# Kernel tuning notes

Measured on AMD Instinct MI355X. Metric: run time of the kernel, lower is better.

The kernel has to match this reference:

```python
import jax, jax.numpy as jnp
import numpy as np

B, S, D, H, ROT = 2, 2048, 2048, 16, 64
HD = D // H  # 128


def setup_inputs() -> dict:
    key = jax.random.key(0)
    ks = jax.random.split(key, 6)
    sc = 0.02
    return {
        "hidden_states": jax.random.normal(ks[0], (B, S, D), jnp.float32),
        "attention_mask": jnp.zeros((B, 1, 1, S), jnp.float32),  # HF additive mask; 0 == keep
        "position_ids": jnp.tile(jnp.arange(S, dtype=jnp.int32), (B, 1)),
        "Wq": jax.random.normal(ks[1], (D, D), jnp.float32) * sc,
        "Wk": jax.random.normal(ks[2], (D, D), jnp.float32) * sc,
        "Wv": jax.random.normal(ks[3], (D, D), jnp.float32) * sc,
        "Wo": jax.random.normal(ks[4], (D, D), jnp.float32) * sc,
        "norm_const": 0.5 * jnp.ones((1, H, 1, 1), jnp.float32),
    }


def _rotate_every_two(x):
    x1 = x[..., ::2]
    x2 = x[..., 1::2]
    return jnp.stack((-x2, x1), axis=-1).reshape(x.shape)


def _apply_rope(x, sin, cos):
    # x: [B,S,H,ROT]; sin/cos: [B,S,ROT//2] -> repeat_interleave(2) as in GPT-J
    sin2 = jnp.repeat(sin, 2, axis=-1)[:, :, None, :]
    cos2 = jnp.repeat(cos, 2, axis=-1)[:, :, None, :]
    return x * cos2 + _rotate_every_two(x) * sin2


def reference(hidden_states, attention_mask, position_ids, Wq, Wk, Wv, Wo, norm_const):
    # projections (nn.Linear, no bias): y = x @ W^T
    q = (hidden_states @ Wq.T).reshape(B, S, H, HD)
    k = (hidden_states @ Wk.T).reshape(B, S, H, HD)
    v = (hidden_states @ Wv.T).reshape(B, S, H, HD).transpose(0, 2, 1, 3)  # [B,H,S,HD]

    # GPT-J sinusoidal rotary on first ROT dims
    inv_freq = 1.0 / (10000.0 ** (jnp.arange(0, ROT, 2, dtype=jnp.float32) / ROT))
    ang = position_ids.astype(jnp.float32)[:, :, None] * inv_freq  # [B,S,ROT//2]
    sin, cos = jnp.sin(ang), jnp.cos(ang)
    q = jnp.concatenate([_apply_rope(q[..., :ROT], sin, cos), q[..., ROT:]], axis=-1)
    k = jnp.concatenate([_apply_rope(k[..., :ROT], sin, cos), k[..., ROT:]], axis=-1)
    q = q.transpose(0, 2, 1, 3)  # [B,H,S,HD]
    k = k.transpose(0, 2, 1, 3)

    # cosine attention: L2-normalize q and k (F.normalize, eps=1e-12)
    eps = 1e-12
    qn = q / jnp.clip(jnp.linalg.norm(q, axis=-1, keepdims=True), eps)
    kn = k / jnp.clip(jnp.linalg.norm(k, axis=-1, keepdims=True), eps)

    keep = attention_mask == 0                               # [B,1,1,S] bool
    causal = jnp.tril(jnp.ones((S, S), bool))[None, None]    # [1,1,S,S]
    # per-query count of visible keys -> value rescale with learned exponent
    counts = jnp.sum((causal & keep).astype(jnp.float32), axis=-1, keepdims=True)  # [B,1,S,1]
    expo = jax.nn.sigmoid(norm_const)                        # [1,H,1,1]
    v = v / jnp.clip(counts ** expo, 1.0)                    # [B,H,S,HD]

    keep_t = jnp.swapaxes(keep, -1, -2).astype(q.dtype)      # [B,1,S,1]
    qn = qn * keep_t
    kn = kn * keep_t
    v = v * keep_t

    attn = jnp.einsum('bhqd,bhkd->bhqk', qn, kn)             # cosine scores
    attn = jnp.where(causal, attn, 0.0)                      # causal zero-mask (no softmax)
    out = jnp.einsum('bhqk,bhkd->bhqd', attn, v)             # [B,H,S,HD]
    out = out.transpose(0, 2, 1, 3).reshape(B, S, D)
    return out @ Wo.T
```

## Files before the change

kernel.cpp:

```cpp
#include <hip/hip_runtime.h>
#include <hip/hip_bf16.h>

typedef __attribute__((ext_vector_type(8))) short bf16x8;
typedef __attribute__((ext_vector_type(4))) float f32x4;
typedef unsigned short u16;
typedef unsigned int u32;

constexpr int B = 2, S = 2048, D = 2048, H = 16, HD = 128, ROT = 64;
constexpr int NQKV = 3 * D;

__device__ __forceinline__ void gload16(const u16* g, u16* l)
{
    __builtin_amdgcn_global_load_lds((const __attribute__((address_space(1))) void*)g,
                                     (__attribute__((address_space(3))) void*)l, 16, 0, 0);
}

__device__ __forceinline__ float bf2f(u32 lo16) { return __uint_as_float(lo16 << 16); }

__global__ void cast_kernel(const float* __restrict__ in, u16* __restrict__ out, int n4)
{
    int idx = blockIdx.x * blockDim.x + threadIdx.x;
    int stride = gridDim.x * blockDim.x;
    for (int i = idx; i < n4; i += stride) {
        float4 v = ((const float4*)in)[i];
        __hip_bfloat16 a = __float2bfloat16(v.x);
        __hip_bfloat16 b = __float2bfloat16(v.y);
        __hip_bfloat16 c = __float2bfloat16(v.z);
        __hip_bfloat16 d = __float2bfloat16(v.w);
        ushort4 o;
        o.x = *(u16*)&a; o.y = *(u16*)&b; o.z = *(u16*)&c; o.w = *(u16*)&d;
        ((ushort4*)out)[i] = o;
    }
}

__global__ void castw_kernel(const float* __restrict__ w0, const float* __restrict__ w1,
                             const float* __restrict__ w2, const float* __restrict__ w3,
                             u16* __restrict__ o0, u16* __restrict__ o1,
                             u16* __restrict__ o2, u16* __restrict__ o3, int n4)
{
    int which = blockIdx.y;
    const float* src = which == 0 ? w0 : which == 1 ? w1 : which == 2 ? w2 : w3;
    u16* dst = which == 0 ? o0 : which == 1 ? o1 : which == 2 ? o2 : o3;
    int idx = blockIdx.x * blockDim.x + threadIdx.x;
    int stride = gridDim.x * blockDim.x;
    for (int i = idx; i < n4; i += stride) {
        float4 v = ((const float4*)src)[i];
        __hip_bfloat16 a = __float2bfloat16(v.x);
        __hip_bfloat16 b = __float2bfloat16(v.y);
        __hip_bfloat16 c = __float2bfloat16(v.z);
        __hip_bfloat16 d = __float2bfloat16(v.w);
        ushort4 o;
        o.x = *(u16*)&a; o.y = *(u16*)&b; o.z = *(u16*)&c; o.w = *(u16*)&d;
        ((ushort4*)dst)[i] = o;
    }
}

__global__ void prep_kernel(const float* __restrict__ mask, const int* __restrict__ pos,
                            const float* __restrict__ ncst,
                            float* __restrict__ sinb, float* __restrict__ cosb,
                            float* __restrict__ keep, float* __restrict__ expo)
{
    int gid = blockIdx.x * blockDim.x + threadIdx.x;
    int total = B * S * 32;
    if (gid < total) {
        int j = gid & 31;
        int bs = gid >> 5;
        float p = (float)pos[bs];
        float f = powf(10000.f, -(float)j / 32.f);
        float ang = p * f;
        sinb[gid] = sinf(ang);
        cosb[gid] = cosf(ang);
        if (j == 0) keep[bs] = (mask[bs] == 0.f) ? 1.f : 0.f;
    }
    if (gid < H) expo[gid] = 1.f / (1.f + expf(-ncst[gid]));
}

__global__ void counts_kernel(const float* __restrict__ keep, float* __restrict__ counts)
{
    __shared__ float part[256];
    int b = blockIdx.x, t = threadIdx.x;
    float v[8];
    float s = 0.f;
    const float* kp = keep + b * S + t * 8;
#pragma unroll
    for (int i = 0; i < 8; ++i) { s += kp[i]; v[i] = s; }
    part[t] = s;
    __syncthreads();
    float off = 0.f;
    for (int j = 0; j < t; ++j) off += part[j];
    float* cp = counts + b * S + t * 8;
#pragma unroll
    for (int i = 0; i < 8; ++i) cp[i] = off + v[i];
}


template <int CNT>
__device__ __forceinline__ void stage_op(const u16* __restrict__ G, int K,
                                         int trow0, int kt, u16* lbuf, int tid)
{
#pragma unroll
    for (int l = 0; l < CNT; ++l) {
        int idx = l * 512 + tid;
        int row = idx >> 2;
        int slot = idx & 3;
        int col8 = slot ^ ((row >> 1) & 3);
        const u16* g = G + (size_t)(trow0 + row) * K + kt * 32 + col8 * 8;
        u16* ld = lbuf + (size_t)(idx & ~63) * 8;
        gload16(g, ld);
    }
}

template <int BM, int BN, int CA, int CB, int MR, int NR, int BF16OUT>
__global__ __launch_bounds__(512, 2) void gemm32(
    const u16* __restrict__ A, const u16* __restrict__ Bm,
    float* __restrict__ Cf, u16* __restrict__ Cb, int N, int K, int ntn)
{
    __shared__ u16 As[3 * BM * 32];
    __shared__ u16 Bs[3 * BN * 32];
    const int tid = threadIdx.x;
    const int lane = tid & 63;
    const int w = tid >> 6;
    const int wm = w >> 2;
    const int wn = w & 3;
    const int l15 = lane & 15, l4 = lane >> 4;

    int nwg = gridDim.x;
    int bid = blockIdx.x;
    int cpx = nwg >> 3;
    int sbid = (bid & 7) * cpx + (bid >> 3);
    int bm = sbid / ntn, bn = sbid % ntn;
    const int bmrow = bm * BM, bnrow = bn * BN;

    f32x4 acc[MR][NR] = {};
    const int nk = K >> 5;

    stage_op<CA>(A, K, bmrow, 0, &As[0], tid);
    stage_op<CB>(Bm, K, bnrow, 0, &Bs[0], tid);
    stage_op<CA>(A, K, bmrow, 1, &As[BM * 32], tid);
    stage_op<CB>(Bm, K, bnrow, 1, &Bs[BN * 32], tid);

    int c0 = 0;
    for (int t = 0; t < nk; ++t) {
        const u16* ab = &As[c0 * BM * 32];
        const u16* bb = &Bs[c0 * BN * 32];
        if (t + 2 < nk) {
            int c2 = c0 + 2; if (c2 >= 3) c2 -= 3;
            stage_op<CA>(A, K, bmrow, t + 2, &As[c2 * BM * 32], tid);
            stage_op<CB>(Bm, K, bnrow, t + 2, &Bs[c2 * BN * 32], tid);
            asm volatile("s_waitcnt vmcnt(%0)" :: "i"(2 * (CA + CB)) : "memory");
        } else if (t + 1 < nk) {
            asm volatile("s_waitcnt vmcnt(%0)" :: "i"(CA + CB) : "memory");
        } else {
            asm volatile("s_waitcnt vmcnt(0)" ::: "memory");
        }
        __builtin_amdgcn_sched_barrier(0);
        __builtin_amdgcn_s_barrier();

        bf16x8 af[MR];
#pragma unroll
        for (int i = 0; i < MR; ++i) {
            int row = wm * (BM / 2) + i * 16 + l15;
            int slot = l4 ^ ((row >> 1) & 3);
            af[i] = *(const bf16x8*)(ab + row * 32 + slot * 8);
        }
#pragma unroll
        for (int n = 0; n < NR; ++n) {
            int brow = wn * (BN / 4) + n * 16 + l15;
            int bslot = l4 ^ ((brow >> 1) & 3);
            bf16x8 bf = *(const bf16x8*)(bb + brow * 32 + bslot * 8);
            __builtin_amdgcn_s_setprio(1);
#pragma unroll
            for (int i = 0; i < MR; ++i)
                acc[i][n] = __builtin_amdgcn_mfma_f32_16x16x32_bf16(af[i], bf, acc[i][n], 0, 0, 0);
            __builtin_amdgcn_s_setprio(0);
        }
        __builtin_amdgcn_sched_barrier(0);
        __builtin_amdgcn_s_barrier();
        c0 = (c0 + 1 == 3) ? 0 : c0 + 1;
    }

#pragma unroll
    for (int i = 0; i < MR; ++i) {
        int row = bmrow + wm * (BM / 2) + i * 16 + l4 * 4;
#pragma unroll
        for (int n = 0; n < NR; ++n) {
            int col = bnrow + wn * (BN / 4) + n * 16 + l15;
            f32x4 v = acc[i][n];
#pragma unroll
            for (int r = 0; r < 4; ++r) {
                if (BF16OUT) {
                    __hip_bfloat16 hv = __float2bfloat16(v[r]);
                    Cb[(size_t)(row + r) * N + col] = *(u16*)&hv;
                } else {
                    Cf[(size_t)(row + r) * N + col] = v[r];
                }
            }
        }
    }
}

__global__ void postproc_all(const u16* __restrict__ tmpb,
                             u16* __restrict__ qn, u16* __restrict__ kn, u16* __restrict__ vr,
                             const float* __restrict__ sinb, const float* __restrict__ cosb,
                             const float* __restrict__ keep, const float* __restrict__ counts,
                             const float* __restrict__ expo)
{
    int gw = (blockIdx.x * blockDim.x + threadIdx.x) >> 6;
    int lane = threadIdx.x & 63;
    if (gw >= B * S * H) return;
    int h = gw % H;
    int sb = gw / H;
    int s = sb % S;
    int b = sb / S;
    const u16* rowp = tmpb + (size_t)(b * S + s) * NQKV;
    u32 qv = *(const u32*)(rowp + h * 128 + lane * 2);
    u32 kv = *(const u32*)(rowp + D + h * 128 + lane * 2);
    u32 vv = *(const u32*)(rowp + 2 * D + h * 128 + lane * 2);
    float q0 = bf2f(qv & 0xffff), q1 = bf2f(qv >> 16);
    float k0 = bf2f(kv & 0xffff), k1 = bf2f(kv >> 16);
    float v0 = bf2f(vv & 0xffff), v1 = bf2f(vv >> 16);
    if (lane < 32) {
        float sn = sinb[(b * S + s) * 32 + lane];
        float cs = cosb[(b * S + s) * 32 + lane];
        float nq0 = q0 * cs - q1 * sn, nq1 = q1 * cs + q0 * sn;
        float nk0 = k0 * cs - k1 * sn, nk1 = k1 * cs + k0 * sn;
        q0 = nq0; q1 = nq1; k0 = nk0; k1 = nk1;
    }
    float sq = q0 * q0 + q1 * q1;
    float sk = k0 * k0 + k1 * k1;
#pragma unroll
    for (int o = 1; o < 64; o <<= 1) {
        sq += __shfl_xor(sq, o, 64);
        sk += __shfl_xor(sk, o, 64);
    }
    float kf = keep[b * S + s];
    float scq = kf / fmaxf(sqrtf(sq), 1e-12f);
    float sck = kf / fmaxf(sqrtf(sk), 1e-12f);
    float cnt = counts[b * S + s];
    float e = expo[h];
    float scv = kf / fmaxf(powf(cnt, e), 1.0f);

    __hip_bfloat16 a0 = __float2bfloat16(q0 * scq), a1 = __float2bfloat16(q1 * scq);
    __hip_bfloat16 b0 = __float2bfloat16(k0 * sck), b1 = __float2bfloat16(k1 * sck);
    __hip_bfloat16 c0 = __float2bfloat16(v0 * scv), c1 = __float2bfloat16(v1 * scv);
    size_t obase = ((size_t)(b * H + h) * S + s) * 128 + lane * 2;
    *(u32*)(qn + obase) = (u32)*(u16*)&a0 | ((u32)*(u16*)&a1 << 16);
    *(u32*)(kn + obase) = (u32)*(u16*)&b0 | ((u32)*(u16*)&b1 << 16);
    *(u32*)(vr + obase) = (u32)*(u16*)&c0 | ((u32)*(u16*)&c1 << 16);
}

__global__ __launch_bounds__(256) void chunk_state(
    const u16* __restrict__ kn, const u16* __restrict__ vr, u16* __restrict__ T16)
{
    __shared__ u16 As[128][72];
    __shared__ u16 Bs[128][72];
    int tid = threadIdx.x, lane = tid & 63, w = tid >> 6;
    int wm = w >> 1, wn = w & 1;
    int c = blockIdx.x, bh = blockIdx.y;
    const int l15 = lane & 15, l4 = lane >> 4;
    size_t base = (size_t)bh * S * 128;
    f32x4 acc[4][4] = {};

    for (int t = 0; t < 2; ++t) {
#pragma unroll
        for (int i = 0; i < 4; ++i) {
            int q = tid + i * 256;
            int r = q >> 4, c16 = q & 15;
            uint4 v = *(const uint4*)(vr + base + (size_t)(c * 128 + t * 64 + r) * 128 + c16 * 8);
            const u16* pv = (const u16*)&v;
#pragma unroll
            for (int j = 0; j < 8; ++j) As[c16 * 8 + j][r] = pv[j];
        }
#pragma unroll
        for (int i = 0; i < 4; ++i) {
            int q = tid + i * 256;
            int r = q >> 4, c16 = q & 15;
            uint4 v = *(const uint4*)(kn + base + (size_t)(c * 128 + t * 64 + r) * 128 + c16 * 8);
            const u16* pv = (const u16*)&v;
#pragma unroll
            for (int j = 0; j < 8; ++j) Bs[c16 * 8 + j][r] = pv[j];
        }
        __syncthreads();
#pragma unroll
        for (int tt = 0; tt < 2; ++tt) {
            bf16x8 a[4], b[4];
#pragma unroll
            for (int m = 0; m < 4; ++m)
                a[m] = *(const bf16x8*)(&As[wm * 64 + m * 16 + l15][tt * 32 + l4 * 8]);
#pragma unroll
            for (int n = 0; n < 4; ++n)
                b[n] = *(const bf16x8*)(&Bs[wn * 64 + n * 16 + l15][tt * 32 + l4 * 8]);
#pragma unroll
            for (int m = 0; m < 4; ++m)
#pragma unroll
                for (int n = 0; n < 4; ++n)
                    acc[m][n] = __builtin_amdgcn_mfma_f32_16x16x32_bf16(a[m], b[n], acc[m][n], 0, 0, 0);
        }
        __syncthreads();
    }
#pragma unroll
    for (int m = 0; m < 4; ++m) {
        int row = wm * 64 + m * 16 + l4 * 4;
#pragma unroll
        for (int n = 0; n < 4; ++n) {
            int col = wn * 64 + n * 16 + l15;
#pragma unroll
            for (int r = 0; r < 4; ++r) {
                __hip_bfloat16 hv = __float2bfloat16(acc[m][n][r]);
                T16[((size_t)(bh * 16 + c) * 128 + row + r) * 128 + col] = *(u16*)&hv;
            }
        }
    }
}

__global__ void prefix_state(const u16* __restrict__ T16, u16* __restrict__ P16)
{
    int g = blockIdx.x * blockDim.x + threadIdx.x;
    int bh = g >> 11;
    int i8 = (g & 2047) * 8;
    const u16* tp = T16 + (size_t)bh * 16 * 16384 + i8;
    u16* pp = P16 + (size_t)bh * 16 * 16384 + i8;
    float run[8] = {};
    for (int c = 0; c < 16; ++c) {
        u16 ob[8];
#pragma unroll
        for (int j = 0; j < 8; ++j) { __hip_bfloat16 hv = __float2bfloat16(run[j]); ob[j] = *(u16*)&hv; }
        *(uint4*)(pp + (size_t)c * 16384) = *(uint4*)ob;
        uint4 tv = *(const uint4*)(tp + (size_t)c * 16384);
        const u16* tvp = (const u16*)&tv;
#pragma unroll
        for (int j = 0; j < 8; ++j) run[j] += bf2f(tvp[j]);
    }
}

__global__ __launch_bounds__(256, 2) void attn2(
    const u16* __restrict__ qn, const u16* __restrict__ kn,
    const u16* __restrict__ vr, const u16* __restrict__ P16, u16* __restrict__ ao)
{
    __shared__ u16 KN[64][136];
    __shared__ u16 VT[128][72];
    __shared__ u16 SC[128][72];
    int tid = threadIdx.x, lane = tid & 63, w = tid >> 6;
    int c = blockIdx.x, bh = blockIdx.y;
    int b = bh >> 4, h = bh & 15;
    const int l15 = lane & 15, l4 = lane >> 4;
    size_t base = (size_t)bh * S * 128;
    const u16* Pp = P16 + (size_t)(bh * 16 + c) * 16384;

    bf16x8 qa[2][4];
#pragma unroll
    for (int m = 0; m < 2; ++m)
#pragma unroll
        for (int t = 0; t < 4; ++t) {
            int row = c * 128 + w * 32 + m * 16 + l15;
            qa[m][t] = *(const bf16x8*)(qn + base + (size_t)row * 128 + t * 32 + l4 * 8);
        }

    f32x4 acc[2][8] = {};

#pragma unroll
    for (int pt = 0; pt < 2; ++pt) {
#pragma unroll
        for (int i = 0; i < 4; ++i) {
            int q = tid + i * 256;
            int r = q >> 3, c8 = q & 7;
            uint4 v = *(const uint4*)(Pp + (size_t)r * 128 + pt * 64 + c8 * 8);
            *(uint4*)(&VT[r][c8 * 8]) = v;
        }
        __syncthreads();
#pragma unroll
        for (int tt = 0; tt < 2; ++tt) {
            bf16x8 pb[8];
#pragma unroll
            for (int n = 0; n < 8; ++n)
                pb[n] = *(const bf16x8*)(&VT[n * 16 + l15][tt * 32 + l4 * 8]);
#pragma unroll
            for (int m = 0; m < 2; ++m)
#pragma unroll
                for (int n = 0; n < 8; ++n)
                    acc[m][n] = __builtin_amdgcn_mfma_f32_16x16x32_bf16(qa[m][pt * 2 + tt], pb[n], acc[m][n], 0, 0, 0);
        }
        __syncthreads();
    }

    for (int kt2 = 0; kt2 < 2; ++kt2) {
#pragma unroll
        for (int i = 0; i < 4; ++i) {
            int q = tid + i * 256;
            int r = q >> 4, c8 = q & 15;
            uint4 v = *(const uint4*)(kn + base + (size_t)(c * 128 + kt2 * 64 + r) * 128 + c8 * 8);
            *(uint4*)(&KN[r][c8 * 8]) = v;
        }
#pragma unroll
        for (int i = 0; i < 4; ++i) {
            int q = tid + i * 256;
            int r = q >> 4, c16 = q & 15;
            uint4 v = *(const uint4*)(vr + base + (size_t)(c * 128 + kt2 * 64 + r) * 128 + c16 * 8);
            const u16* pv = (const u16*)&v;
#pragma unroll
            for (int j = 0; j < 8; ++j) VT[c16 * 8 + j][r] = pv[j];
        }
        __syncthreads();
        f32x4 sacc[2][4] = {};
#pragma unroll
        for (int t = 0; t < 4; ++t) {
            bf16x8 kb[4];
#pragma unroll
            for (int n = 0; n < 4; ++n)
                kb[n] = *(const bf16x8*)(&KN[n * 16 + l15][t * 32 + l4 * 8]);
#pragma unroll
            for (int m = 0; m < 2; ++m)
#pragma unroll
                for (int n = 0; n < 4; ++n)
                    sacc[m][n] = __builtin_amdgcn_mfma_f32_16x16x32_bf16(qa[m][t], kb[n], sacc[m][n], 0, 0, 0);
        }
#pragma unroll
        for (int m = 0; m < 2; ++m)
#pragma unroll
            for (int n = 0; n < 4; ++n)
#pragma unroll
                for (int r = 0; r < 4; ++r) {
                    int rowl = w * 32 + m * 16 + l4 * 4 + r;
                    int coll = n * 16 + l15;
                    int kl = kt2 * 64 + coll;
                    float val = (kl <= rowl) ? sacc[m][n][r] : 0.f;
                    __hip_bfloat16 hv = __float2bfloat16(val);
                    SC[rowl][coll] = *(u16*)&hv;
                }
#pragma unroll
        for (int t = 0; t < 2; ++t) {
            bf16x8 sa[2], vb[8];
#pragma unroll
            for (int m = 0; m < 2; ++m)
                sa[m] = *(const bf16x8*)(&SC[w * 32 + m * 16 + l15][t * 32 + l4 * 8]);
#pragma unroll
            for (int n = 0; n < 8; ++n)
                vb[n] = *(const bf16x8*)(&VT[n * 16 + l15][t * 32 + l4 * 8]);
#pragma unroll
            for (int m = 0; m < 2; ++m)
#pragma unroll
                for (int n = 0; n < 8; ++n)
                    acc[m][n] = __builtin_amdgcn_mfma_f32_16x16x32_bf16(sa[m], vb[n], acc[m][n], 0, 0, 0);
        }
        __syncthreads();
    }

#pragma unroll
    for (int m = 0; m < 2; ++m)
#pragma unroll
        for (int n = 0; n < 8; ++n)
#pragma unroll
            for (int r = 0; r < 4; ++r) {
                int srow = c * 128 + w * 32 + m * 16 + l4 * 4 + r;
                int d = n * 16 + l15;
                __hip_bfloat16 hv = __float2bfloat16(acc[m][n][r]);
                ao[(size_t)(b * S + srow) * D + h * 128 + d] = *(u16*)&hv;
            }
}

extern "C" void kernel_launch(void* const* d_in, const int* in_sizes, int n_in,
                              void* d_out, int out_size, void* d_ws, size_t ws_size,
                              hipStream_t stream)
{
    const float* hs = (const float*)d_in[0];
    const float* mask = (const float*)d_in[1];
    const int* pos = (const int*)d_in[2];
    const float* Wq = (const float*)d_in[3];
    const float* Wk = (const float*)d_in[4];
    const float* Wv = (const float*)d_in[5];
    const float* Wo = (const float*)d_in[6];
    const float* ncst = (const float*)d_in[7];
    float* out = (float*)d_out;

    char* ws = (char*)d_ws;
    size_t off = 0;
    auto alloc = [&](size_t bytes) {
        size_t o = off;
        off += (bytes + 255) & ~(size_t)255;
        return o;
    };
    u16* hs16 = (u16*)(ws + alloc((size_t)B * S * D * 2));
    u16* wqkv16 = (u16*)(ws + alloc((size_t)NQKV * D * 2));
    u16* wo16 = (u16*)(ws + alloc((size_t)D * D * 2));
    u16* tmpb = (u16*)(ws + alloc((size_t)B * S * NQKV * 2));
    u16* qn16 = (u16*)(ws + alloc((size_t)B * S * D * 2));
    u16* kn16 = (u16*)(ws + alloc((size_t)B * S * D * 2));
    u16* vr16 = (u16*)(ws + alloc((size_t)B * S * D * 2));
    float* sinb = (float*)(ws + alloc((size_t)B * S * 32 * 4));
    float* cosb = (float*)(ws + alloc((size_t)B * S * 32 * 4));
    float* keep = (float*)(ws + alloc((size_t)B * S * 4));
    float* counts = (float*)(ws + alloc((size_t)B * S * 4));
    float* expo = (float*)(ws + alloc(64));
    u16* ao16 = tmpb;
    u16* T16 = tmpb + (size_t)8388608;
    u16* P16 = tmpb + (size_t)16777216;

    cast_kernel<<<2048, 256, 0, stream>>>(hs, hs16, B * S * D / 4);
    castw_kernel<<<dim3(512, 4), 256, 0, stream>>>(
        Wq, Wk, Wv, Wo,
        wqkv16, wqkv16 + (size_t)D * D, wqkv16 + (size_t)2 * D * D, wo16, D * D / 4);
    prep_kernel<<<(B * S * 32 + 255) / 256, 256, 0, stream>>>(mask, pos, ncst, sinb, cosb, keep, expo);
    counts_kernel<<<B, 256, 0, stream>>>(keep, counts);

    gemm32<256, 384, 2, 3, 8, 6, 1><<<256, 512, 0, stream>>>(
        hs16, wqkv16, nullptr, tmpb, NQKV, D, NQKV / 384);

    postproc_all<<<(B * S * H) / 4, 256, 0, stream>>>(tmpb, qn16, kn16, vr16, sinb, cosb, keep, counts, expo);

    dim3 gc(S / 128, B * H);
    chunk_state<<<gc, 256, 0, stream>>>(kn16, vr16, T16);
    prefix_state<<<256, 256, 0, stream>>>(T16, P16);
    attn2<<<gc, 256, 0, stream>>>(qn16, kn16, vr16, P16, ao16);

    gemm32<128, 256, 1, 2, 4, 4, 0><<<256, 512, 0, stream>>>(
        ao16, wo16, out, nullptr, D, D, D / 256);
}
```

Baseline: 282.8 us.

## Fuse RoPE, L2-normalize and value rescale into QKV GEMM epilogue; merge prep kernels

The QKV GEMM epilogue now applies rotary embedding on the fp32 accumulators using lane shuffles. It computes per-head squared norms through shared-memory partial sums, scales q/k/v, and writes bf16 directly in the head-major layout. This removes the bf16 round trip through a temporary QKV buffer and the separate postproc kernel. The four small prep and cast kernels are merged into one launch, with sin/cos packed as float2. The risks are a heavier epilogue with scattered 2-byte stores and extra register pressure in the GEMM.

```diff
diff --git a/kernel.cpp b/kernel.cpp
--- a/kernel.cpp
+++ b/kernel.cpp
@@ -17,80 +17,64 @@
 
 __device__ __forceinline__ float bf2f(u32 lo16) { return __uint_as_float(lo16 << 16); }
 
-__global__ void cast_kernel(const float* __restrict__ in, u16* __restrict__ out, int n4)
-{
-    int idx = blockIdx.x * blockDim.x + threadIdx.x;
-    int stride = gridDim.x * blockDim.x;
-    for (int i = idx; i < n4; i += stride) {
-        float4 v = ((const float4*)in)[i];
-        __hip_bfloat16 a = __float2bfloat16(v.x);
-        __hip_bfloat16 b = __float2bfloat16(v.y);
-        __hip_bfloat16 c = __float2bfloat16(v.z);
-        __hip_bfloat16 d = __float2bfloat16(v.w);
-        ushort4 o;
-        o.x = *(u16*)&a; o.y = *(u16*)&b; o.z = *(u16*)&c; o.w = *(u16*)&d;
-        ((ushort4*)out)[i] = o;
-    }
-}
-
-__global__ void castw_kernel(const float* __restrict__ w0, const float* __restrict__ w1,
-                             const float* __restrict__ w2, const float* __restrict__ w3,
-                             u16* __restrict__ o0, u16* __restrict__ o1,
-                             u16* __restrict__ o2, u16* __restrict__ o3, int n4)
-{
-    int which = blockIdx.y;
-    const float* src = which == 0 ? w0 : which == 1 ? w1 : which == 2 ? w2 : w3;
-    u16* dst = which == 0 ? o0 : which == 1 ? o1 : which == 2 ? o2 : o3;
-    int idx = blockIdx.x * blockDim.x + threadIdx.x;
-    int stride = gridDim.x * blockDim.x;
-    for (int i = idx; i < n4; i += stride) {
-        float4 v = ((const float4*)src)[i];
-        __hip_bfloat16 a = __float2bfloat16(v.x);
-        __hip_bfloat16 b = __float2bfloat16(v.y);
-        __hip_bfloat16 c = __float2bfloat16(v.z);
-        __hip_bfloat16 d = __float2bfloat16(v.w);
-        ushort4 o;
-        o.x = *(u16*)&a; o.y = *(u16*)&b; o.z = *(u16*)&c; o.w = *(u16*)&d;
-        ((ushort4*)dst)[i] = o;
-    }
-}
-
-__global__ void prep_kernel(const float* __restrict__ mask, const int* __restrict__ pos,
-                            const float* __restrict__ ncst,
-                            float* __restrict__ sinb, float* __restrict__ cosb,
-                            float* __restrict__ keep, float* __restrict__ expo)
-{
-    int gid = blockIdx.x * blockDim.x + threadIdx.x;
-    int total = B * S * 32;
-    if (gid < total) {
+__global__ void fused_prep(const float* __restrict__ hs,
+                           const float* __restrict__ Wq, const float* __restrict__ Wk,
+                           const float* __restrict__ Wv, const float* __restrict__ Wo,
+                           const float* __restrict__ mask, const int* __restrict__ pos,
+                           const float* __restrict__ ncst,
+                           u16* __restrict__ hs16, u16* __restrict__ wqkv16, u16* __restrict__ wo16,
+                           float2* __restrict__ sc2, float* __restrict__ keep,
+                           float* __restrict__ expo, float* __restrict__ counts)
+{
+    int bid = blockIdx.x, tid = threadIdx.x;
+    if (bid < 1024) {
+        const int total = 2097152 + 4 * 1048576;
+        int idx = bid * 256 + tid;
+        int stride = 1024 * 256;
+        for (int i = idx; i < total; i += stride) {
+            const float* src; u16* dst; int off;
+            if (i < 2097152) { src = hs; dst = hs16; off = i; }
+            else {
+                int j = i - 2097152;
+                int wsel = j >> 20; off = j & 1048575;
+                src = wsel == 0 ? Wq : wsel == 1 ? Wk : wsel == 2 ? Wv : Wo;
+                dst = wsel < 3 ? wqkv16 + (size_t)wsel * D * D : wo16;
+            }
+            float4 v = ((const float4*)src)[off];
+            __hip_bfloat16 a = __float2bfloat16(v.x);
+            __hip_bfloat16 b = __float2bfloat16(v.y);
+            __hip_bfloat16 c = __float2bfloat16(v.z);
+            __hip_bfloat16 d = __float2bfloat16(v.w);
+            ushort4 o;
+            o.x = *(u16*)&a; o.y = *(u16*)&b; o.z = *(u16*)&c; o.w = *(u16*)&d;
+            ((ushort4*)dst)[off] = o;
+        }
+    } else if (bid < 1536) {
+        int gid = (bid - 1024) * 256 + tid;
         int j = gid & 31;
         int bs = gid >> 5;
         float p = (float)pos[bs];
         float f = powf(10000.f, -(float)j / 32.f);
         float ang = p * f;
-        sinb[gid] = sinf(ang);
-        cosb[gid] = cosf(ang);
+        sc2[gid] = make_float2(cosf(ang), sinf(ang));
         if (j == 0) keep[bs] = (mask[bs] == 0.f) ? 1.f : 0.f;
-    }
-    if (gid < H) expo[gid] = 1.f / (1.f + expf(-ncst[gid]));
-}
-
-__global__ void counts_kernel(const float* __restrict__ keep, float* __restrict__ counts)
-{
-    __shared__ float part[256];
-    int b = blockIdx.x, t = threadIdx.x;
-    float v[8];
-    float s = 0.f;
-    const float* kp = keep + b * S + t * 8;
-#pragma unroll
-    for (int i = 0; i < 8; ++i) { s += kp[i]; v[i] = s; }
-    part[t] = s;
-    __syncthreads();
-    float off = 0.f;
-    for (int j = 0; j < t; ++j) off += part[j];
-    float* cp = counts + b * S + t * 8;
-#pragma unroll
-    for (int i = 0; i < 8; ++i) cp[i] = off + v[i];
+        if (gid < H) expo[gid] = 1.f / (1.f + expf(-ncst[gid]));
+    } else {
+        __shared__ float part[256];
+        int b = bid - 1536, t = tid;
+        float v[8];
+        float s = 0.f;
+        const float* mp = mask + b * S + t * 8;
+#pragma unroll
+        for (int i = 0; i < 8; ++i) { s += (mp[i] == 0.f) ? 1.f : 0.f; v[i] = s; }
+        part[t] = s;
+        __syncthreads();
+        float off = 0.f;
+        for (int j = 0; j < t; ++j) off += part[j];
+        float* cp = counts + b * S + t * 8;
+#pragma unroll
+        for (int i = 0; i < 8; ++i) cp[i] = off + v[i];
+    }
 }
 
 
@@ -110,11 +94,14 @@
     }
 }
 
-template <int BM, int BN, int CA, int CB, int MR, int NR, int BF16OUT>
-__global__ __launch_bounds__(512, 2) void gemm32(
+__global__ __launch_bounds__(512, 2) void gemm_qkv(
     const u16* __restrict__ A, const u16* __restrict__ Bm,
-    float* __restrict__ Cf, u16* __restrict__ Cb, int N, int K, int ntn)
-{
+    u16* __restrict__ qn, u16* __restrict__ kn, u16* __restrict__ vr,
+    const float* __restrict__ keep, const float* __restrict__ counts,
+    const float* __restrict__ expo, const float2* __restrict__ sc2)
+{
+    constexpr int BM = 256, BN = 384, CA = 2, CB = 3, MR = 8, NR = 6;
+    const int K = D, ntn = NQKV / BN;
     __shared__ u16 As[3 * BM * 32];
     __shared__ u16 Bs[3 * BN * 32];
     const int tid = threadIdx.x;
@@ -179,6 +166,180 @@
         c0 = (c0 + 1 == 3) ? 0 : c0 + 1;
     }
 
+    float* ps = (float*)&As[0];
+    float* psc = ps + 3072;
+    for (int z = tid; z < 3072; z += 512) ps[z] = 0.f;
+    __syncthreads();
+
+    const int hbmin = (wn * 96) >> 7;
+    float ss[MR][4][2];
+#pragma unroll
+    for (int i = 0; i < MR; ++i)
+#pragma unroll
+        for (int r = 0; r < 4; ++r) { ss[i][r][0] = 0.f; ss[i][r][1] = 0.f; }
+
+#pragma unroll
+    for (int i = 0; i < MR; ++i)
+#pragma unroll
+        for (int n = 0; n < NR; ++n) {
+            int gcol_n = bnrow + wn * 96 + n * 16;
+            int ty = gcol_n >> 11;
+            int dloc = gcol_n & 127;
+            int hslot = ((wn * 96 + n * 16) >> 7) - hbmin;
+            bool dorope = (ty < 2) && (dloc < 64);
+#pragma unroll
+            for (int r = 0; r < 4; ++r) {
+                float v = acc[i][n][r];
+                float pv = __shfl_xor(v, 1, 64);
+                if (dorope) {
+                    int row = bmrow + wm * 128 + i * 16 + l4 * 4 + r;
+                    float2 cs = sc2[row * 32 + ((dloc + l15) >> 1)];
+                    v = (l15 & 1) ? (v * cs.x + pv * cs.y) : (v * cs.x - pv * cs.y);
+                    acc[i][n][r] = v;
+                }
+                if (ty < 2) ss[i][r][hslot] += v * v;
+            }
+        }
+
+#pragma unroll
+    for (int i = 0; i < MR; ++i)
+#pragma unroll
+        for (int r = 0; r < 4; ++r)
+#pragma unroll
+            for (int tt = 0; tt < 2; ++tt) {
+                float x = ss[i][r][tt];
+                x += __shfl_xor(x, 1, 64);
+                x += __shfl_xor(x, 2, 64);
+                x += __shfl_xor(x, 4, 64);
+                x += __shfl_xor(x, 8, 64);
+                ss[i][r][tt] = x;
+            }
+    if (l15 == 0) {
+#pragma unroll
+        for (int i = 0; i < MR; ++i)
+#pragma unroll
+            for (int r = 0; r < 4; ++r)
+#pragma unroll
+                for (int tt = 0; tt < 2; ++tt) {
+                    int hb = hbmin + tt;
+                    if (hb < 3) ps[(wm * 128 + i * 16 + l4 * 4 + r) * 12 + hb * 4 + wn] = ss[i][r][tt];
+                }
+    }
+    __syncthreads();
+
+    if (tid < 256) {
+        int row = bmrow + tid;
+        float kf = keep[row];
+        float cnt = counts[row];
+#pragma unroll
+        for (int hb = 0; hb < 3; ++hb) {
+            int gcol = bnrow + hb * 128;
+            int ty = gcol >> 11;
+            int gh = (gcol >> 7) & 15;
+            float sc;
+            if (ty == 2) {
+                sc = kf / fmaxf(powf(cnt, expo[gh]), 1.f);
+            } else {
+                float sum = ps[tid * 12 + hb * 4 + 0] + ps[tid * 12 + hb * 4 + 1] +
+                            ps[tid * 12 + hb * 4 + 2] + ps[tid * 12 + hb * 4 + 3];
+                sc = kf / fmaxf(sqrtf(sum), 1e-12f);
+            }
+            psc[tid * 3 + hb] = sc;
+        }
+    }
+    __syncthreads();
+
+#pragma unroll
+    for (int i = 0; i < MR; ++i)
+#pragma unroll
+        for (int r = 0; r < 4; ++r) {
+            int rowl = wm * 128 + i * 16 + l4 * 4 + r;
+            int row = bmrow + rowl;
+            int b2 = row >> 11, s = row & 2047;
+#pragma unroll
+            for (int n = 0; n < NR; ++n) {
+                int gcol_n = bnrow + wn * 96 + n * 16;
+                int ty = gcol_n >> 11;
+                int gh = (gcol_n >> 7) & 15;
+                int dloc = gcol_n & 127;
+                int hb = (wn * 96 + n * 16) >> 7;
+                float v = acc[i][n][r] * psc[rowl * 3 + hb];
+                __hip_bfloat16 hv = __float2bfloat16(v);
+                u16* dst = ty == 0 ? qn : ty == 1 ? kn : vr;
+                dst[((size_t)(b2 * 16 + gh) * 2048 + s) * 128 + dloc + l15] = *(u16*)&hv;
+            }
+        }
+}
+
+template <int BM, int BN, int CA, int CB, int MR, int NR>
+__global__ __launch_bounds__(512, 2) void gemm32(
+    const u16* __restrict__ A, const u16* __restrict__ Bm,
+    float* __restrict__ Cf, int N, int K, int ntn)
+{
+    __shared__ u16 As[3 * BM * 32];
+    __shared__ u16 Bs[3 * BN * 32];
+    const int tid = threadIdx.x;
+    const int lane = tid & 63;
+    const int w = tid >> 6;
+    const int wm = w >> 2;
+    const int wn = w & 3;
+    const int l15 = lane & 15, l4 = lane >> 4;
+
+    int nwg = gridDim.x;
+    int bid = blockIdx.x;
+    int cpx = nwg >> 3;
+    int sbid = (bid & 7) * cpx + (bid >> 3);
+    int bm = sbid / ntn, bn = sbid % ntn;
+    const int bmrow = bm * BM, bnrow = bn * BN;
+
+    f32x4 acc[MR][NR] = {};
+    const int nk = K >> 5;
+
+    stage_op<CA>(A, K, bmrow, 0, &As[0], tid);
+    stage_op<CB>(Bm, K, bnrow, 0, &Bs[0], tid);
+    stage_op<CA>(A, K, bmrow, 1, &As[BM * 32], tid);
+    stage_op<CB>(Bm, K, bnrow, 1, &Bs[BN * 32], tid);
+
+    int c0 = 0;
+    for (int t = 0; t < nk; ++t) {
+        const u16* ab = &As[c0 * BM * 32];
+        const u16* bb = &Bs[c0 * BN * 32];
+        if (t + 2 < nk) {
+            int c2 = c0 + 2; if (c2 >= 3) c2 -= 3;
+            stage_op<CA>(A, K, bmrow, t + 2, &As[c2 * BM * 32], tid);
+            stage_op<CB>(Bm, K, bnrow, t + 2, &Bs[c2 * BN * 32], tid);
+            asm volatile("s_waitcnt vmcnt(%0)" :: "i"(2 * (CA + CB)) : "memory");
+        } else if (t + 1 < nk) {
+            asm volatile("s_waitcnt vmcnt(%0)" :: "i"(CA + CB) : "memory");
+        } else {
+            asm volatile("s_waitcnt vmcnt(0)" ::: "memory");
+        }
+        __builtin_amdgcn_sched_barrier(0);
+        __builtin_amdgcn_s_barrier();
+
+        bf16x8 af[MR];
+#pragma unroll
+        for (int i = 0; i < MR; ++i) {
+            int row = wm * (BM / 2) + i * 16 + l15;
+            int slot = l4 ^ ((row >> 1) & 3);
+            af[i] = *(const bf16x8*)(ab + row * 32 + slot * 8);
+        }
+#pragma unroll
+        for (int n = 0; n < NR; ++n) {
+            int brow = wn * (BN / 4) + n * 16 + l15;
+            int bslot = l4 ^ ((brow >> 1) & 3);
+            bf16x8 bf = *(const bf16x8*)(bb + brow * 32 + bslot * 8);
+            __builtin_amdgcn_s_setprio(1);
+#pragma unroll
+            for (int i = 0; i < MR; ++i)
+                acc[i][n] = __builtin_amdgcn_mfma_f32_16x16x32_bf16(af[i], bf, acc[i][n], 0, 0, 0);
+            __builtin_amdgcn_s_setprio(0);
+        }
+        __builtin_amdgcn_sched_barrier(0);
+        __builtin_amdgcn_s_barrier();
+        c0 = (c0 + 1 == 3) ? 0 : c0 + 1;
+    }
+
 #pragma unroll
     for (int i = 0; i < MR; ++i) {
         int row = bmrow + wm * (BM / 2) + i * 16 + l4 * 4;
@@ -187,66 +348,10 @@
             int col = bnrow + wn * (BN / 4) + n * 16 + l15;
             f32x4 v = acc[i][n];
 #pragma unroll
-            for (int r = 0; r < 4; ++r) {
-                if (BF16OUT) {
-                    __hip_bfloat16 hv = __float2bfloat16(v[r]);
-                    Cb[(size_t)(row + r) * N + col] = *(u16*)&hv;
-                } else {
-                    Cf[(size_t)(row + r) * N + col] = v[r];
-                }
-            }
-        }
-    }
-}
-
-__global__ void postproc_all(const u16* __restrict__ tmpb,
-                             u16* __restrict__ qn, u16* __restrict__ kn, u16* __restrict__ vr,
-                             const float* __restrict__ sinb, const float* __restrict__ cosb,
-                             const float* __restrict__ keep, const float* __restrict__ counts,
-                             const float* __restrict__ expo)
-{
-    int gw = (blockIdx.x * blockDim.x + threadIdx.x) >> 6;
-    int lane = threadIdx.x & 63;
-    if (gw >= B * S * H) return;
-    int h = gw % H;
-    int sb = gw / H;
-    int s = sb % S;
-    int b = sb / S;
-    const u16* rowp = tmpb + (size_t)(b * S + s) * NQKV;
-    u32 qv = *(const u32*)(rowp + h * 128 + lane * 2);
-    u32 kv = *(const u32*)(rowp + D + h * 128 + lane * 2);
-    u32 vv = *(const u32*)(rowp + 2 * D + h * 128 + lane * 2);
-    float q0 = bf2f(qv & 0xffff), q1 = bf2f(qv >> 16);
-    float k0 = bf2f(kv & 0xffff), k1 = bf2f(kv >> 16);
-    float v0 = bf2f(vv & 0xffff), v1 = bf2f(vv >> 16);
-    if (lane < 32) {
-        float sn = sinb[(b * S + s) * 32 + lane];
-        float cs = cosb[(b * S + s) * 32 + lane];
-        float nq0 = q0 * cs - q1 * sn, nq1 = q1 * cs + q0 * sn;
-        float nk0 = k0 * cs - k1 * sn, nk1 = k1 * cs + k0 * sn;
-        q0 = nq0; q1 = nq1; k0 = nk0; k1 = nk1;
-    }
-    float sq = q0 * q0 + q1 * q1;
-    float sk = k0 * k0 + k1 * k1;
-#pragma unroll
-    for (int o = 1; o < 64; o <<= 1) {
-        sq += __shfl_xor(sq, o, 64);
-        sk += __shfl_xor(sk, o, 64);
-    }
-    float kf = keep[b * S + s];
-    float scq = kf / fmaxf(sqrtf(sq), 1e-12f);
-    float sck = kf / fmaxf(sqrtf(sk), 1e-12f);
-    float cnt = counts[b * S + s];
-    float e = expo[h];
-    float scv = kf / fmaxf(powf(cnt, e), 1.0f);
-
-    __hip_bfloat16 a0 = __float2bfloat16(q0 * scq), a1 = __float2bfloat16(q1 * scq);
-    __hip_bfloat16 b0 = __float2bfloat16(k0 * sck), b1 = __float2bfloat16(k1 * sck);
-    __hip_bfloat16 c0 = __float2bfloat16(v0 * scv), c1 = __float2bfloat16(v1 * scv);
-    size_t obase = ((size_t)(b * H + h) * S + s) * 128 + lane * 2;
-    *(u32*)(qn + obase) = (u32)*(u16*)&a0 | ((u32)*(u16*)&a1 << 16);
-    *(u32*)(kn + obase) = (u32)*(u16*)&b0 | ((u32)*(u16*)&b1 << 16);
-    *(u32*)(vr + obase) = (u32)*(u16*)&c0 | ((u32)*(u16*)&c1 << 16);
+            for (int r = 0; r < 4; ++r)
+                Cf[(size_t)(row + r) * N + col] = v[r];
+        }
+    }
 }
 
 __global__ __launch_bounds__(256) void chunk_state(
@@ -482,36 +587,29 @@
     u16* hs16 = (u16*)(ws + alloc((size_t)B * S * D * 2));
     u16* wqkv16 = (u16*)(ws + alloc((size_t)NQKV * D * 2));
     u16* wo16 = (u16*)(ws + alloc((size_t)D * D * 2));
-    u16* tmpb = (u16*)(ws + alloc((size_t)B * S * NQKV * 2));
+    u16* scratch = (u16*)(ws + alloc((size_t)B * S * NQKV * 2));
     u16* qn16 = (u16*)(ws + alloc((size_t)B * S * D * 2));
     u16* kn16 = (u16*)(ws + alloc((size_t)B * S * D * 2));
     u16* vr16 = (u16*)(ws + alloc((size_t)B * S * D * 2));
-    float* sinb = (float*)(ws + alloc((size_t)B * S * 32 * 4));
-    float* cosb = (float*)(ws + alloc((size_t)B * S * 32 * 4));
+    float2* sc2 = (float2*)(ws + alloc((size_t)B * S * 32 * 8));
     float* keep = (float*)(ws + alloc((size_t)B * S * 4));
     float* counts = (float*)(ws + alloc((size_t)B * S * 4));
     float* expo = (float*)(ws + alloc(64));
-    u16* ao16 = tmpb;
-    u16* T16 = tmpb + (size_t)8388608;
-    u16* P16 = tmpb + (size_t)16777216;
-
-    cast_kernel<<<2048, 256, 0, stream>>>(hs, hs16, B * S * D / 4);
-    castw_kernel<<<dim3(512, 4), 256, 0, stream>>>(
-        Wq, Wk, Wv, Wo,
-        wqkv16, wqkv16 + (size_t)D * D, wqkv16 + (size_t)2 * D * D, wo16, D * D / 4);
-    prep_kernel<<<(B * S * 32 + 255) / 256, 256, 0, stream>>>(mask, pos, ncst, sinb, cosb, keep, expo);
-    counts_kernel<<<B, 256, 0, stream>>>(keep, counts);
-
-    gemm32<256, 384, 2, 3, 8, 6, 1><<<256, 512, 0, stream>>>(
-        hs16, wqkv16, nullptr, tmpb, NQKV, D, NQKV / 384);
-
-    postproc_all<<<(B * S * H) / 4, 256, 0, stream>>>(tmpb, qn16, kn16, vr16, sinb, cosb, keep, counts, expo);
+    u16* ao16 = scratch;
+    u16* T16 = scratch + (size_t)8388608;
+    u16* P16 = scratch + (size_t)16777216;
+
+    fused_prep<<<1538, 256, 0, stream>>>(hs, Wq, Wk, Wv, Wo, mask, pos, ncst,
+                                         hs16, wqkv16, wo16, sc2, keep, expo, counts);
+
+    gemm_qkv<<<256, 512, 0, stream>>>(hs16, wqkv16, qn16, kn16, vr16,
+                                      keep, counts, expo, sc2);
 
     dim3 gc(S / 128, B * H);
     chunk_state<<<gc, 256, 0, stream>>>(kn16, vr16, T16);
     prefix_state<<<256, 256, 0, stream>>>(T16, P16);
     attn2<<<gc, 256, 0, stream>>>(qn16, kn16, vr16, P16, ao16);
 
-    gemm32<128, 256, 1, 2, 4, 4, 0><<<256, 512, 0, stream>>>(
-        ao16, wo16, out, nullptr, D, D, D / 256);
-}
+    gemm32<128, 256, 1, 2, 4, 4><<<256, 512, 0, stream>>>(
+        ao16, wo16, out, D, D, D / 256);
+}
```

After: 352.5 us. 24.7% more time.
